# Optimization experiments

Hardware: AMD Instinct MI355X
Metric: run time of the kernel (lower is better)

## Reference

```python
import jax, jax.numpy as jnp
import numpy as np


def setup_inputs() -> dict:
    key = jax.random.key(0)
    k1, k2 = jax.random.split(key)
    B, C, N = 8, 3, 4096
    ori_pcs = jax.random.normal(k1, (B, C, N), dtype=jnp.float32)
    adv_pcs = jax.random.normal(k2, (B, C, N), dtype=jnp.float32)
    return {"ori_pcs": ori_pcs, "adv_pcs": adv_pcs}


def _chamfer(ori_pcs, adv_pcs, single=False, reduce="max"):
    # [B, 3, N] -> [B, N, 3]
    x = jnp.swapaxes(ori_pcs, 1, 2)
    y = jnp.swapaxes(adv_pcs, 1, 2)
    x2 = jnp.sum(x * x, axis=-1)  # [B, N]
    y2 = jnp.sum(y * y, axis=-1)  # [B, M]
    # squared pairwise distances [B, N, M]
    d = x2[:, :, None] + y2[:, None, :] - 2.0 * jnp.einsum("bnd,bmd->bnm", x, y)
    d = jnp.maximum(d, 0.0)
    d1 = jnp.mean(jnp.min(d, axis=2), axis=1)  # ori -> adv, per batch [B]
    if single:
        return jnp.mean(d1)
    d2 = jnp.mean(jnp.min(d, axis=1), axis=1)  # adv -> ori, per batch [B]
    if reduce == "max":
        per_batch = jnp.maximum(d1, d2)
    else:  # 'sum' / 'mean' style fallback
        per_batch = d1 + d2
    return jnp.mean(per_batch)


def reference(ori_pcs, adv_pcs):
    return _chamfer(ori_pcs, adv_pcs, single=False, reduce="max")
```

## Files before the change

### kernel.cpp

```cpp
#include <hip/hip_runtime.h>
#include <float.h>

#define BATCH 8
#define NPTS 4096
#define BLK 512
#define THALF 1024
#define NH 4
#define NRG 8

typedef __attribute__((ext_vector_type(8))) short short8;
typedef __attribute__((ext_vector_type(16))) float floatx16;

union U4S8 { uint4 u; short8 s; };
__device__ inline short8 asS8(uint4 u) { U4S8 t; t.u = u; return t.s; }

__device__ inline unsigned short f2bf(float f) {
    unsigned u = __float_as_uint(f);
    return (unsigned short)((u + 0x7FFFu + ((u >> 16) & 1u)) >> 16);
}
__device__ inline float bf2f(unsigned short h) {
    return __uint_as_float(((unsigned)h) << 16);
}
__device__ inline unsigned flag_token(int i) {
    return 0x9E3779B9u * (unsigned)(i + 7);
}

#define SBAR() __builtin_amdgcn_sched_barrier(0)

__global__ __launch_bounds__(BLK, 4) void chamfer_partial(
        const float* __restrict__ ori, const float* __restrict__ adv,
        float* __restrict__ rfin) {
    __shared__ uint4 fr[2 * THALF];

    int bx = blockIdx.x;
    int half = bx & (NH - 1);
    int rowgroup = (bx >> 2) & (NRG - 1);
    int dirb = bx >> 5;
    int b = dirb & 7;
    int dir = dirb >> 3;

    const float* qsrc = dir ? adv : ori;
    const float* tsrc = dir ? ori : adv;

    {
        const float* tx = tsrc + (b * 3 + 0) * NPTS;
        const float* ty = tsrc + (b * 3 + 1) * NPTS;
        const float* tz = tsrc + (b * 3 + 2) * NPTS;
        #pragma unroll
        for (int i = 0; i < THALF / BLK; ++i) {
            int p = threadIdx.x + i * BLK;
            int m = half * THALF + p;
            float x = tx[m], y = ty[m], z = tz[m];
            float n2 = fmaf(x, x, fmaf(y, y, z * z));
            unsigned short hx = f2bf(x), hy = f2bf(y), hz = f2bf(z);
            unsigned short lx = f2bf(x - bf2f(hx));
            unsigned short ly = f2bf(y - bf2f(hy));
            unsigned short lz = f2bf(z - bf2f(hz));
            unsigned short h2 = f2bf(n2);
            unsigned short l2 = f2bf(n2 - bf2f(h2));
            uint4 v0;
            v0.x = (unsigned)hx | ((unsigned)hy << 16);
            v0.y = (unsigned)hz | ((unsigned)lx << 16);
            v0.z = (unsigned)ly | ((unsigned)lz << 16);
            v0.w = (unsigned)h2 | ((unsigned)l2 << 16);
            uint4 v1;
            v1.x = v0.x;
            v1.y = (unsigned)hz | (0x3F80u << 16);
            v1.z = 0x00003F80u;
            v1.w = 0u;
            fr[p] = v0;
            fr[THALF + p] = v1;
        }
    }

    int w = threadIdx.x >> 6;
    int l = threadIdx.x & 63;
    int lrow = l & 31;
    int kh = l >> 5;

    short8 afrag0, afrag1;
    #pragma unroll
    for (int bi = 0; bi < 2; ++bi) {
        int q = rowgroup * 512 + (w * 2 + bi) * 32 + lrow;
        float x = qsrc[(b * 3 + 0) * NPTS + q];
        float y = qsrc[(b * 3 + 1) * NPTS + q];
        float z = qsrc[(b * 3 + 2) * NPTS + q];
        float n2 = fmaf(x, x, fmaf(y, y, z * z));
        unsigned short hx = f2bf(x), hy = f2bf(y), hz = f2bf(z);
        unsigned short lx = f2bf(x - bf2f(hx));
        unsigned short ly = f2bf(y - bf2f(hy));
        unsigned short lz = f2bf(z - bf2f(hz));
        unsigned short h2 = f2bf(n2);
        unsigned short l2 = f2bf(n2 - bf2f(h2));
        unsigned short mhx = f2bf(-2.0f * bf2f(hx));
        unsigned short mhy = f2bf(-2.0f * bf2f(hy));
        unsigned short mhz = f2bf(-2.0f * bf2f(hz));
        unsigned short mlx = f2bf(-2.0f * bf2f(lx));
        unsigned short mly = f2bf(-2.0f * bf2f(ly));
        unsigned short mlz = f2bf(-2.0f * bf2f(lz));
        const unsigned short one = 0x3F80;
        union { unsigned short us[8]; short8 s8; } A;
        if (kh == 0) {
            A.us[0] = mhx; A.us[1] = mhy; A.us[2] = mhz;
            A.us[3] = mhx; A.us[4] = mhy; A.us[5] = mhz;
            A.us[6] = one; A.us[7] = one;
        } else {
            A.us[0] = mlx; A.us[1] = mly; A.us[2] = mlz;
            A.us[3] = h2;  A.us[4] = l2;
            A.us[5] = 0;   A.us[6] = 0;   A.us[7] = 0;
        }
        if (bi == 0) afrag0 = A.s8; else afrag1 = A.s8;
    }
    __syncthreads();

    floatx16 zero, rmn0, rmn1;
    #pragma unroll
    for (int r = 0; r < 16; ++r) { zero[r] = 0.0f; rmn0[r] = FLT_MAX; rmn1[r] = FLT_MAX; }

    const uint4* tp = fr + kh * THALF + lrow;

    {
        uint4 f0 = tp[0], f1 = tp[1 << 5];
        floatx16 a0 = __builtin_amdgcn_mfma_f32_32x32x16_bf16(afrag0, asS8(f0), zero, 0, 0, 0);
        floatx16 a1 = __builtin_amdgcn_mfma_f32_32x32x16_bf16(afrag0, asS8(f1), zero, 0, 0, 0);
        uint4 fn0 = tp[2 << 5], fn1 = tp[3 << 5];
        #pragma unroll
        for (int r = 0; r < 16; ++r)
            rmn0[r] = fminf(fminf(rmn0[r], a0[r]), a1[r]);
        floatx16 c0 = __builtin_amdgcn_mfma_f32_32x32x16_bf16(afrag1, asS8(f0), zero, 0, 0, 0);
        floatx16 c1 = __builtin_amdgcn_mfma_f32_32x32x16_bf16(afrag1, asS8(f1), zero, 0, 0, 0);
        f0 = fn0; f1 = fn1;

        #pragma unroll 1
        for (int ct = 2; ct < 32; ct += 2) {
            #pragma unroll
            for (int r = 0; r < 16; ++r)
                rmn1[r] = fminf(fminf(rmn1[r], c0[r]), c1[r]);
            SBAR();
            a0 = __builtin_amdgcn_mfma_f32_32x32x16_bf16(afrag0, asS8(f0), zero, 0, 0, 0);
            a1 = __builtin_amdgcn_mfma_f32_32x32x16_bf16(afrag0, asS8(f1), zero, 0, 0, 0);
            SBAR();
            int nt = (ct + 2) & 31;
            fn0 = tp[nt << 5]; fn1 = tp[(nt + 1) << 5];
            SBAR();
            #pragma unroll
            for (int r = 0; r < 16; ++r)
                rmn0[r] = fminf(fminf(rmn0[r], a0[r]), a1[r]);
            SBAR();
            c0 = __builtin_amdgcn_mfma_f32_32x32x16_bf16(afrag1, asS8(f0), zero, 0, 0, 0);
            c1 = __builtin_amdgcn_mfma_f32_32x32x16_bf16(afrag1, asS8(f1), zero, 0, 0, 0);
            SBAR();
            f0 = fn0; f1 = fn1;
        }
        #pragma unroll
        for (int r = 0; r < 16; ++r)
            rmn1[r] = fminf(fminf(rmn1[r], c0[r]), c1[r]);
    }

    bool b0 = (l & 1), b1 = (l & 2), b2 = (l & 4), b3 = (l & 8);

#define FOLD(v)                                                                \
    {                                                                          \
        _Pragma("unroll")                                                      \
        for (int i = 0; i < 8; ++i) {                                          \
            float send = b0 ? v[i] : v[i + 8];                                 \
            float recv = __shfl_xor(send, 1);                                  \
            v[i] = fminf(b0 ? v[i + 8] : v[i], recv);                          \
        }                                                                      \
        _Pragma("unroll")                                                      \
        for (int i = 0; i < 4; ++i) {                                          \
            float send = b1 ? v[i] : v[i + 4];                                 \
            float recv = __shfl_xor(send, 2);                                  \
            v[i] = fminf(b1 ? v[i + 4] : v[i], recv);                          \
        }                                                                      \
        _Pragma("unroll")                                                      \
        for (int i = 0; i < 2; ++i) {                                          \
            float send = b2 ? v[i] : v[i + 2];                                 \
            float recv = __shfl_xor(send, 4);                                  \
            v[i] = fminf(b2 ? v[i + 2] : v[i], recv);                          \
        }                                                                      \
        {                                                                      \
            float send = b3 ? v[0] : v[1];                                     \
            float recv = __shfl_xor(send, 8);                                  \
            v[0] = fminf(b3 ? v[1] : v[0], recv);                              \
        }                                                                      \
        v[0] = fminf(v[0], __shfl_xor(v[0], 16));                              \
    }

    FOLD(rmn0);
    FOLD(rmn1);
#undef FOLD

    if ((l & 16) == 0) {
        int g = l & 15;
        int rr = ((g & 1) << 3) | ((g & 2) << 1) | ((g & 4) >> 1) | ((g & 8) >> 3);
        int rowin = (rr & 3) + 8 * (rr >> 2) + 4 * kh;
        float* base = rfin + (((size_t)(dirb * NH + half)) << 12)
                    + rowgroup * 512;
        base[(w * 2 + 0) * 32 + rowin] = rmn0[0];
        base[(w * 2 + 1) * 32 + rowin] = rmn1[0];
    }
}

__global__ __launch_bounds__(256) void combine_kernel(
        const float* __restrict__ rfin, float* __restrict__ pb,
        unsigned* __restrict__ flags, float* __restrict__ out) {
    __shared__ float ws[4];
    __shared__ float sh[64 + 16];
    int cb = blockIdx.x;
    int dirb = cb >> 2, slice = cb & 3;
    const float* p = rfin + (((size_t)dirb * NH) << 12);
    float s = 0.0f;
    #pragma unroll
    for (int k = 0; k < 4; ++k) {
        int row = slice * 1024 + k * 256 + threadIdx.x;
        float m = fminf(fminf(p[row], p[(1 << 12) + row]),
                        fminf(p[(2 << 12) + row], p[(3 << 12) + row]));
        s += fmaxf(m, 0.0f);
    }
    for (int off = 32; off > 0; off >>= 1) s += __shfl_down(s, off);
    int wid = threadIdx.x >> 6, lane = threadIdx.x & 63;
    if (lane == 0) ws[wid] = s;
    __syncthreads();
    if (threadIdx.x == 0) {
        float t = ws[0] + ws[1] + ws[2] + ws[3];
        atomicExch((unsigned*)(pb + cb), __float_as_uint(t));
        __threadfence();
        atomicExch(flags + cb, flag_token(cb));
    }

    if (cb == 0) {
        __syncthreads();
        int t = threadIdx.x;
        if (t < 64) {
            unsigned want = flag_token(t);
            while (atomicAdd(flags + t, 0u) != want) {
                __builtin_amdgcn_s_sleep(1);
            }
            sh[t] = __uint_as_float(atomicAdd((unsigned*)(pb + t), 0u));
        }
        __syncthreads();
        if (t < 16) {
            sh[64 + t] = sh[t * 4] + sh[t * 4 + 1] + sh[t * 4 + 2] + sh[t * 4 + 3];
        }
        __syncthreads();
        if (t == 0) {
            float acc = 0.0f;
            #pragma unroll
            for (int bb = 0; bb < BATCH; ++bb)
                acc += fmaxf(sh[64 + bb], sh[64 + 8 + bb]);
            out[0] = acc * (1.0f / (float)NPTS) * (1.0f / (float)BATCH);
        }
    }
}

extern "C" void kernel_launch(void* const* d_in, const int* in_sizes, int n_in,
                              void* d_out, int out_size, void* d_ws, size_t ws_size,
                              hipStream_t stream) {
    const float* ori = (const float*)d_in[0];
    const float* adv = (const float*)d_in[1];
    float* out = (float*)d_out;

    float* rfin = (float*)d_ws;
    float* pb = rfin + (size_t)16 * NH * NPTS;
    unsigned* flags = (unsigned*)(pb + 64);

    chamfer_partial<<<16 * NRG * NH, BLK, 0, stream>>>(ori, adv, rfin);
    combine_kernel<<<64, 256, 0, stream>>>(rfin, pb, flags, out);
}
```

Baseline: 19.06 us.

## Compute both chamfer directions from one distance matrix via row and column mins

Instead of computing the distance matrix twice (ori->adv and adv->ori), each block computes one tile of the ori-vs-adv matrix and reduces it along rows and along columns. Column minima are tree-reduced in registers, folded across the two half-waves, and combined across warps through shared memory into a cpart buffer. The combine kernel is widened to reduce 8 partials per direction. This roughly halves MFMA work in exchange for extra per-tile reduction ALU work, LDS traffic and an additional barrier.

```diff
diff --git a/kernel.cpp b/kernel.cpp
--- a/kernel.cpp
+++ b/kernel.cpp
@@ -4,8 +4,8 @@
 #define BATCH 8
 #define NPTS 4096
 #define BLK 512
-#define THALF 1024
-#define NH 4
+#define TOCT 512
+#define NOCT 8
 #define NRG 8
 
 typedef __attribute__((ext_vector_type(8))) short short8;
@@ -27,50 +27,51 @@
 
 #define SBAR() __builtin_amdgcn_sched_barrier(0)
 
-__global__ __launch_bounds__(BLK, 4) void chamfer_partial(
+__device__ inline float tree16(const floatx16& v) {
+    float t0 = fminf(fminf(v[0], v[1]), fminf(v[2], v[3]));
+    float t1 = fminf(fminf(v[4], v[5]), fminf(v[6], v[7]));
+    float t2 = fminf(fminf(v[8], v[9]), fminf(v[10], v[11]));
+    float t3 = fminf(fminf(v[12], v[13]), fminf(v[14], v[15]));
+    return fminf(fminf(t0, t1), fminf(t2, t3));
+}
+
+__global__ __launch_bounds__(BLK, 4) void chamfer_sym(
         const float* __restrict__ ori, const float* __restrict__ adv,
-        float* __restrict__ rfin) {
-    __shared__ uint4 fr[2 * THALF];
+        float* __restrict__ rpart, float* __restrict__ cpart) {
+    __shared__ uint4 fr[2 * TOCT];
+    __shared__ float cmin[8][TOCT];
 
     int bx = blockIdx.x;
-    int half = bx & (NH - 1);
-    int rowgroup = (bx >> 2) & (NRG - 1);
-    int dirb = bx >> 5;
-    int b = dirb & 7;
-    int dir = dirb >> 3;
-
-    const float* qsrc = dir ? adv : ori;
-    const float* tsrc = dir ? ori : adv;
+    int oct = bx & (NOCT - 1);
+    int rg  = (bx >> 3) & (NRG - 1);
+    int b   = bx >> 6;
 
     {
-        const float* tx = tsrc + (b * 3 + 0) * NPTS;
-        const float* ty = tsrc + (b * 3 + 1) * NPTS;
-        const float* tz = tsrc + (b * 3 + 2) * NPTS;
-        #pragma unroll
-        for (int i = 0; i < THALF / BLK; ++i) {
-            int p = threadIdx.x + i * BLK;
-            int m = half * THALF + p;
-            float x = tx[m], y = ty[m], z = tz[m];
-            float n2 = fmaf(x, x, fmaf(y, y, z * z));
-            unsigned short hx = f2bf(x), hy = f2bf(y), hz = f2bf(z);
-            unsigned short lx = f2bf(x - bf2f(hx));
-            unsigned short ly = f2bf(y - bf2f(hy));
-            unsigned short lz = f2bf(z - bf2f(hz));
-            unsigned short h2 = f2bf(n2);
-            unsigned short l2 = f2bf(n2 - bf2f(h2));
-            uint4 v0;
-            v0.x = (unsigned)hx | ((unsigned)hy << 16);
-            v0.y = (unsigned)hz | ((unsigned)lx << 16);
-            v0.z = (unsigned)ly | ((unsigned)lz << 16);
-            v0.w = (unsigned)h2 | ((unsigned)l2 << 16);
-            uint4 v1;
-            v1.x = v0.x;
-            v1.y = (unsigned)hz | (0x3F80u << 16);
-            v1.z = 0x00003F80u;
-            v1.w = 0u;
-            fr[p] = v0;
-            fr[THALF + p] = v1;
-        }
+        const float* tx = adv + (b * 3 + 0) * NPTS;
+        const float* ty = adv + (b * 3 + 1) * NPTS;
+        const float* tz = adv + (b * 3 + 2) * NPTS;
+        int p = threadIdx.x;
+        int m = oct * TOCT + p;
+        float x = tx[m], y = ty[m], z = tz[m];
+        float n2 = fmaf(x, x, fmaf(y, y, z * z));
+        unsigned short hx = f2bf(x), hy = f2bf(y), hz = f2bf(z);
+        unsigned short lx = f2bf(x - bf2f(hx));
+        unsigned short ly = f2bf(y - bf2f(hy));
+        unsigned short lz = f2bf(z - bf2f(hz));
+        unsigned short h2 = f2bf(n2);
+        unsigned short l2 = f2bf(n2 - bf2f(h2));
+        uint4 v0;
+        v0.x = (unsigned)hx | ((unsigned)hy << 16);
+        v0.y = (unsigned)hz | ((unsigned)lx << 16);
+        v0.z = (unsigned)ly | ((unsigned)lz << 16);
+        v0.w = (unsigned)h2 | ((unsigned)l2 << 16);
+        uint4 v1;
+        v1.x = v0.x;
+        v1.y = (unsigned)hz | (0x3F80u << 16);
+        v1.z = 0x00003F80u;
+        v1.w = 0u;
+        fr[p] = v0;
+        fr[TOCT + p] = v1;
     }
 
     int w = threadIdx.x >> 6;
@@ -81,10 +82,10 @@
     short8 afrag0, afrag1;
     #pragma unroll
     for (int bi = 0; bi < 2; ++bi) {
-        int q = rowgroup * 512 + (w * 2 + bi) * 32 + lrow;
-        float x = qsrc[(b * 3 + 0) * NPTS + q];
-        float y = qsrc[(b * 3 + 1) * NPTS + q];
-        float z = qsrc[(b * 3 + 2) * NPTS + q];
+        int q = rg * 512 + (w * 2 + bi) * 32 + lrow;
+        float x = ori[(b * 3 + 0) * NPTS + q];
+        float y = ori[(b * 3 + 1) * NPTS + q];
+        float z = ori[(b * 3 + 2) * NPTS + q];
         float n2 = fmaf(x, x, fmaf(y, y, z * z));
         unsigned short hx = f2bf(x), hy = f2bf(y), hz = f2bf(z);
         unsigned short lx = f2bf(x - bf2f(hx));
@@ -117,7 +118,8 @@
     #pragma unroll
     for (int r = 0; r < 16; ++r) { zero[r] = 0.0f; rmn0[r] = FLT_MAX; rmn1[r] = FLT_MAX; }
 
-    const uint4* tp = fr + kh * THALF + lrow;
+    const uint4* tp = fr + kh * TOCT + lrow;
+    float* cmw = cmin[w];
 
     {
         uint4 f0 = tp[0], f1 = tp[1 << 5];
@@ -127,25 +129,35 @@
         #pragma unroll
         for (int r = 0; r < 16; ++r)
             rmn0[r] = fminf(fminf(rmn0[r], a0[r]), a1[r]);
+        float ca0 = tree16(a0), ca1 = tree16(a1);
         floatx16 c0 = __builtin_amdgcn_mfma_f32_32x32x16_bf16(afrag1, asS8(f0), zero, 0, 0, 0);
         floatx16 c1 = __builtin_amdgcn_mfma_f32_32x32x16_bf16(afrag1, asS8(f1), zero, 0, 0, 0);
         f0 = fn0; f1 = fn1;
 
         #pragma unroll 1
-        for (int ct = 2; ct < 32; ct += 2) {
+        for (int ct = 2; ct < 16; ct += 2) {
             #pragma unroll
             for (int r = 0; r < 16; ++r)
                 rmn1[r] = fminf(fminf(rmn1[r], c0[r]), c1[r]);
+            float cc0 = fminf(ca0, tree16(c0));
+            float cc1 = fminf(ca1, tree16(c1));
+            cc0 = fminf(cc0, __shfl_xor(cc0, 32));
+            cc1 = fminf(cc1, __shfl_xor(cc1, 32));
+            if (l < 32) {
+                cmw[((ct - 2) << 5) + l] = cc0;
+                cmw[((ct - 1) << 5) + l] = cc1;
+            }
             SBAR();
             a0 = __builtin_amdgcn_mfma_f32_32x32x16_bf16(afrag0, asS8(f0), zero, 0, 0, 0);
             a1 = __builtin_amdgcn_mfma_f32_32x32x16_bf16(afrag0, asS8(f1), zero, 0, 0, 0);
             SBAR();
-            int nt = (ct + 2) & 31;
+            int nt = (ct + 2) & 15;
             fn0 = tp[nt << 5]; fn1 = tp[(nt + 1) << 5];
             SBAR();
             #pragma unroll
             for (int r = 0; r < 16; ++r)
                 rmn0[r] = fminf(fminf(rmn0[r], a0[r]), a1[r]);
+            ca0 = tree16(a0); ca1 = tree16(a1);
             SBAR();
             c0 = __builtin_amdgcn_mfma_f32_32x32x16_bf16(afrag1, asS8(f0), zero, 0, 0, 0);
             c1 = __builtin_amdgcn_mfma_f32_32x32x16_bf16(afrag1, asS8(f1), zero, 0, 0, 0);
@@ -155,6 +167,14 @@
         #pragma unroll
         for (int r = 0; r < 16; ++r)
             rmn1[r] = fminf(fminf(rmn1[r], c0[r]), c1[r]);
+        float cc0 = fminf(ca0, tree16(c0));
+        float cc1 = fminf(ca1, tree16(c1));
+        cc0 = fminf(cc0, __shfl_xor(cc0, 32));
+        cc1 = fminf(cc1, __shfl_xor(cc1, 32));
+        if (l < 32) {
+            cmw[(14 << 5) + l] = cc0;
+            cmw[(15 << 5) + l] = cc1;
+        }
     }
 
     bool b0 = (l & 1), b1 = (l & 2), b2 = (l & 4), b3 = (l & 8);
@@ -195,27 +215,40 @@
         int g = l & 15;
         int rr = ((g & 1) << 3) | ((g & 2) << 1) | ((g & 4) >> 1) | ((g & 8) >> 3);
         int rowin = (rr & 3) + 8 * (rr >> 2) + 4 * kh;
-        float* base = rfin + (((size_t)(dirb * NH + half)) << 12)
-                    + rowgroup * 512;
+        float* base = rpart + (((size_t)(b * NOCT + oct)) << 12) + rg * 512;
         base[(w * 2 + 0) * 32 + rowin] = rmn0[0];
         base[(w * 2 + 1) * 32 + rowin] = rmn1[0];
     }
+
+    __syncthreads();
+    {
+        int c = threadIdx.x;
+        float m = cmin[0][c];
+        #pragma unroll
+        for (int ww = 1; ww < 8; ++ww) m = fminf(m, cmin[ww][c]);
+        cpart[(((size_t)(b * NRG + rg)) << 12) + oct * TOCT + c] = m;
+    }
 }
 
 __global__ __launch_bounds__(256) void combine_kernel(
-        const float* __restrict__ rfin, float* __restrict__ pb,
-        unsigned* __restrict__ flags, float* __restrict__ out) {
+        const float* __restrict__ rpart, const float* __restrict__ cpart,
+        float* __restrict__ pb, unsigned* __restrict__ flags,
+        float* __restrict__ out) {
     __shared__ float ws[4];
-    __shared__ float sh[64 + 16];
+    __shared__ float sh[128 + 16];
     int cb = blockIdx.x;
-    int dirb = cb >> 2, slice = cb & 3;
-    const float* p = rfin + (((size_t)dirb * NH) << 12);
+    int d2 = cb >> 6;
+    int idx = cb & 63;
+    int b = idx >> 3, slice = idx & 7;
+    const float* p = (d2 ? cpart : rpart) + ((size_t)(b * 8) << 12);
     float s = 0.0f;
     #pragma unroll
-    for (int k = 0; k < 4; ++k) {
-        int row = slice * 1024 + k * 256 + threadIdx.x;
-        float m = fminf(fminf(p[row], p[(1 << 12) + row]),
-                        fminf(p[(2 << 12) + row], p[(3 << 12) + row]));
+    for (int k = 0; k < 2; ++k) {
+        int e = slice * 512 + k * 256 + threadIdx.x;
+        float m = p[e];
+        #pragma unroll
+        for (int pl = 1; pl < 8; ++pl)
+            m = fminf(m, p[((size_t)pl << 12) + e]);
         s += fmaxf(m, 0.0f);
     }
     for (int off = 32; off > 0; off >>= 1) s += __shfl_down(s, off);
@@ -232,7 +265,7 @@
     if (cb == 0) {
         __syncthreads();
         int t = threadIdx.x;
-        if (t < 64) {
+        if (t < 128) {
             unsigned want = flag_token(t);
             while (atomicAdd(flags + t, 0u) != want) {
                 __builtin_amdgcn_s_sleep(1);
@@ -241,14 +274,18 @@
         }
         __syncthreads();
         if (t < 16) {
-            sh[64 + t] = sh[t * 4] + sh[t * 4 + 1] + sh[t * 4 + 2] + sh[t * 4 + 3];
+            int half = t >> 3, bb = t & 7;
+            float a = 0.0f;
+            #pragma unroll
+            for (int ss = 0; ss < 8; ++ss) a += sh[half * 64 + bb * 8 + ss];
+            sh[128 + half * 8 + bb] = a;
         }
         __syncthreads();
         if (t == 0) {
             float acc = 0.0f;
             #pragma unroll
             for (int bb = 0; bb < BATCH; ++bb)
-                acc += fmaxf(sh[64 + bb], sh[64 + 8 + bb]);
+                acc += fmaxf(sh[128 + bb], sh[128 + 8 + bb]);
             out[0] = acc * (1.0f / (float)NPTS) * (1.0f / (float)BATCH);
         }
     }
@@ -261,10 +298,11 @@
     const float* adv = (const float*)d_in[1];
     float* out = (float*)d_out;
 
-    float* rfin = (float*)d_ws;
-    float* pb = rfin + (size_t)16 * NH * NPTS;
-    unsigned* flags = (unsigned*)(pb + 64);
-
-    chamfer_partial<<<16 * NRG * NH, BLK, 0, stream>>>(ori, adv, rfin);
-    combine_kernel<<<64, 256, 0, stream>>>(rfin, pb, flags, out);
-}
+    float* rpart = (float*)d_ws;
+    float* cpart = rpart + (size_t)BATCH * NOCT * NPTS;
+    float* pb = cpart + (size_t)BATCH * NRG * NPTS;
+    unsigned* flags = (unsigned*)(pb + 128);
+
+    chamfer_sym<<<BATCH * NRG * NOCT, BLK, 0, stream>>>(ori, adv, rpart, cpart);
+    combine_kernel<<<128, 256, 0, stream>>>(rpart, cpart, pb, flags, out);
+}
```

New measurement: 21.95 us. +15.1%, slower.
